# Optimization experiments

Measured on AMD Instinct MI355X. Metric: run time of the kernel, lower is better.

## Reference

```python
import jax, jax.numpy as jnp
import numpy as np

N_NODES = 8192
N_EDGES = 65536
NB = 10            # number_of_basis
MID = 32           # middle_layer_size
MAX_R = 10.0       # max_radius
NZ, NM = 48, 16    # z / mol embedding sizes -> 64x0e node input
IN_S = NZ + NM     # 64 scalars
H_S, H_V = 32, 8   # hidden irreps 32x0e + 8x1o (dim 56)
O_S = 16           # output irreps 16x0e
W0N = IN_S * H_S + IN_S * H_V                                  # 2560
W1N = H_S*H_S + H_V*H_S + H_S*H_V + H_V*H_V + H_V*H_V          # 1664
W2N = H_S*O_S + H_V*O_S                                        # 640
H_DIM = H_S + 3 * H_V                                          # 56


def _fcnet(e, W1, W2):
    # e3nn FullyConnectedNet([NB, MID, numel], silu): fan-in normalized linears
    h = jax.nn.silu(e @ W1 / np.sqrt(W1.shape[0]))
    return h @ W2 / np.sqrt(W2.shape[0])


def _ln(x, g, b):
    m = jnp.mean(x, -1, keepdims=True)
    v = jnp.var(x, -1, keepdims=True)
    return (x - m) * jax.lax.rsqrt(v + 1e-5) * g + b


def _sus(t):
    # smooth compact-support bump helper: exp(-1/t) for t>0 else 0
    return jnp.where(t > 0, jnp.exp(-1.0 / jnp.where(t > 0, t, 1.0)), 0.0)


def _forward(pos, Ez, Em,
             b0_W1, b0_W2, b0_g, b0_b,
             b1_W1, b1_W2, b1_g, b1_b,
             b2_W1, b2_W2, b2_g, b2_b,
             z, mol_id, edge_src, edge_dst):
    N = pos.shape[0]
    E = edge_src.shape[0]
    avg = E / N  # avg_num_neighbors (static)

    # node embedding: 64x0e
    x = jnp.concatenate([Ez[z], Em[mol_id]], axis=-1)          # [N, 64]

    vec = pos[edge_dst] - pos[edge_src]                        # [E, 3]
    length = jnp.linalg.norm(vec, axis=1)                      # [E]

    # soft_one_hot_linspace(basis='smooth_finite', cutoff=True) * sqrt(NB)
    vals = jnp.linspace(0.0, MAX_R, NB + 2)[1:-1]
    step = MAX_R / (NB + 1)
    u = (length[:, None] - vals) / step
    emb = (1.14136 * np.exp(2.0)) * _sus(u + 1.0) * _sus(1.0 - u)
    emb = emb * np.sqrt(NB)                                    # [E, NB]

    # spherical harmonics lmax=1, normalize=True, 'component' norm
    nrm = vec / jnp.maximum(length, 1e-9)[:, None]
    sh_v = np.sqrt(3.0) * nrm                                  # [E, 3]  (l=1; l=0 comp == 1)

    # ---- interaction block 0: 64x0e -> 32x0e + 8x1o ----
    w = _fcnet(emb, b0_W1, b0_W2)                              # [E, 2560]
    w00 = w[:, :IN_S * H_S].reshape(E, IN_S, H_S)
    w01 = w[:, IN_S * H_S:].reshape(E, IN_S, H_V)
    xe = x[edge_src]                                           # [E, 64]
    es = jnp.einsum('eu,euw->ew', xe, w00) / np.sqrt(IN_S)
    ev = jnp.einsum('eu,euw,ei->ewi', xe, w01, sh_v) / np.sqrt(IN_S)
    msg = jnp.concatenate([es, ev.reshape(E, 3 * H_V)], -1)    # [E, 56]
    x = _ln(jax.ops.segment_sum(msg, edge_dst, num_segments=N) / np.sqrt(avg), b0_g, b0_b)

    # ---- interaction block 1: 32x0e+8x1o -> 32x0e+8x1o ----
    w = _fcnet(emb, b1_W1, b1_W2)                              # [E, 1664]
    o = 0
    w_ss  = w[:, o:o + H_S*H_S].reshape(E, H_S, H_S); o += H_S*H_S
    w_vvs = w[:, o:o + H_V*H_S].reshape(E, H_V, H_S); o += H_V*H_S
    w_sv  = w[:, o:o + H_S*H_V].reshape(E, H_S, H_V); o += H_S*H_V
    w_vs  = w[:, o:o + H_V*H_V].reshape(E, H_V, H_V); o += H_V*H_V
    w_vvv = w[:, o:o + H_V*H_V].reshape(E, H_V, H_V)
    xs = x[:, :H_S][edge_src]                                  # [E, 32]
    xv = x[:, H_S:].reshape(N, H_V, 3)[edge_src]               # [E, 8, 3]
    dot = jnp.einsum('eui,ei->eu', xv, sh_v) / np.sqrt(3.0)    # 1o x 1o -> 0e CG
    crs = jnp.cross(xv, sh_v[:, None, :]) / np.sqrt(2.0)       # 1o x 1o -> 1o CG
    es = (jnp.einsum('eu,euw->ew', xs, w_ss) / np.sqrt(H_S)
          + jnp.einsum('eu,euw->ew', dot, w_vvs) / np.sqrt(H_V)) / np.sqrt(2.0)
    ev = (jnp.einsum('eu,euw,ei->ewi', xs, w_sv, sh_v) / np.sqrt(H_S)
          + jnp.einsum('eui,euw->ewi', xv, w_vs) / np.sqrt(H_V)
          + jnp.einsum('eui,euw->ewi', crs, w_vvv) / np.sqrt(H_V)) / np.sqrt(3.0)
    msg = jnp.concatenate([es, ev.reshape(E, 3 * H_V)], -1)
    x = _ln(jax.ops.segment_sum(msg, edge_dst, num_segments=N) / np.sqrt(avg), b1_g, b1_b)

    # ---- interaction block 2: 32x0e+8x1o -> 16x0e ----
    w = _fcnet(emb, b2_W1, b2_W2)                              # [E, 640]
    w_ss  = w[:, :H_S * O_S].reshape(E, H_S, O_S)
    w_vvs = w[:, H_S * O_S:].reshape(E, H_V, O_S)
    xs = x[:, :H_S][edge_src]
    xv = x[:, H_S:].reshape(N, H_V, 3)[edge_src]
    dot = jnp.einsum('eui,ei->eu', xv, sh_v) / np.sqrt(3.0)
    es = (jnp.einsum('eu,euw->ew', xs, w_ss) / np.sqrt(H_S)
          + jnp.einsum('eu,euw->ew', dot, w_vvs) / np.sqrt(H_V)) / np.sqrt(2.0)
    x = _ln(jax.ops.segment_sum(es, edge_dst, num_segments=N) / np.sqrt(avg), b2_g, b2_b)
    return x                                                   # [N, 16]


def setup_inputs():
    key = jax.random.key(0)
    ks = jax.random.split(key, 16)
    edge_src = jax.random.randint(ks[3], (N_EDGES,), 0, N_NODES)
    # exclude self-loops (radius_graph never returns them)
    edge_dst = (edge_src + 1 + jax.random.randint(ks[4], (N_EDGES,), 0, N_NODES - 1)) % N_NODES
    return {
        'pos': jax.random.uniform(ks[0], (N_NODES, 3), jnp.float32) * 8.0,
        'z': jax.random.randint(ks[1], (N_NODES,), 0, 100),
        'mol_id': jax.random.randint(ks[2], (N_NODES,), 0, 2),
        'edge_src': edge_src,
        'edge_dst': edge_dst,
        'Ez': jax.random.normal(ks[5], (100, NZ), jnp.float32),
        'Em': jax.random.normal(ks[6], (2, NM), jnp.float32),
        'b0_W1': jax.random.normal(ks[7], (NB, MID), jnp.float32),
        'b0_W2': jax.random.normal(ks[8], (MID, W0N), jnp.float32),
        'b0_g': jnp.ones((H_DIM,), jnp.float32),
        'b0_b': jnp.zeros((H_DIM,), jnp.float32),
        'b1_W1': jax.random.normal(ks[9], (NB, MID), jnp.float32),
        'b1_W2': jax.random.normal(ks[10], (MID, W1N), jnp.float32),
        'b1_g': jnp.ones((H_DIM,), jnp.float32),
        'b1_b': jnp.zeros((H_DIM,), jnp.float32),
        'b2_W1': jax.random.normal(ks[11], (NB, MID), jnp.float32),
        'b2_W2': jax.random.normal(ks[12], (MID, W2N), jnp.float32),
        'b2_g': jnp.ones((O_S,), jnp.float32),
        'b2_b': jnp.zeros((O_S,), jnp.float32),
    }


def reference(pos, z, mol_id, edge_src, edge_dst, Ez, Em,
              b0_W1, b0_W2, b0_g, b0_b,
              b1_W1, b1_W2, b1_g, b1_b,
              b2_W1, b2_W2, b2_g, b2_b):
    return _forward(pos, Ez, Em,
                    b0_W1, b0_W2, b0_g, b0_b,
                    b1_W1, b1_W2, b1_g, b1_b,
                    b2_W1, b2_W2, b2_g, b2_b,
                    z, mol_id, edge_src, edge_dst)
```

## Files before the change

kernel.cpp:

```cpp
#include <hip/hip_runtime.h>

#define NNODES 8192
#define NEDGES 65536

#define K_PACK   0.02209708691f
#define K_P1SV   0.01804219593f
#define K_VVS    0.04419417382f
#define K_VS     0.03608439182f
#define K_VVV    0.02551551815f
#define K_DOT    0.57735026919f
#define K_PRELN  0.35355339059f
#define C_EMB    8.4335730689f

typedef unsigned int uint32;
typedef unsigned short ushort16;
typedef __attribute__((ext_vector_type(8))) short short8;
typedef __attribute__((ext_vector_type(4))) float floatx4;

__device__ __forceinline__ float siluf(float x) { return x / (1.0f + __expf(-x)); }
__device__ __forceinline__ float susf(float t) { return t > 0.0f ? __expf(-1.0f / t) : 0.0f; }
__device__ __forceinline__ ushort16 f2bf(float f) {
  uint32 u = __float_as_uint(f);
  return (ushort16)((u + 0x7fffu + ((u >> 16) & 1u)) >> 16);
}
__device__ __forceinline__ float bflo(uint32 v) { return __uint_as_float(v << 16); }
__device__ __forceinline__ float bfhi(uint32 v) { return __uint_as_float(v & 0xffff0000u); }
__device__ __forceinline__ float bfs(ushort16 v) { return __uint_as_float((uint32)v << 16); }

__global__ __launch_bounds__(256) void k_prep(
    const float* __restrict__ pos, const int* __restrict__ z, const int* __restrict__ mol,
    const int* __restrict__ esrc, const int* __restrict__ edst,
    const float* __restrict__ Ez, const float* __restrict__ Em,
    const float* __restrict__ W10, const float* __restrict__ W11, const float* __restrict__ W12,
    const float* __restrict__ W20, const float* __restrict__ W21, const float* __restrict__ W22,
    int* __restrict__ combo, ushort16* __restrict__ X0cb, float* __restrict__ sh,
    ushort16* __restrict__ h0b, ushort16* __restrict__ h1b, ushort16* __restrict__ h2b,
    ushort16* __restrict__ Bp0, ushort16* __restrict__ Bp1, ushort16* __restrict__ Bp2,
    ushort16* __restrict__ Bpw1, ushort16* __restrict__ Bpw2,
    int* __restrict__ deg, int* __restrict__ eidx) {
  __shared__ float Wl[320];
  int b = blockIdx.x;
  if (b < 768) {
    int which = b >> 8;
    int e = ((b & 255) << 8) + threadIdx.x;
    const float* W = (which == 0) ? W10 : (which == 1) ? W11 : W12;
    for (int i = threadIdx.x; i < 320; i += 256) Wl[i] = W[i];
    __syncthreads();
    int s = esrc[e], d = edst[e];
    float vx = pos[d * 3 + 0] - pos[s * 3 + 0];
    float vy = pos[d * 3 + 1] - pos[s * 3 + 1];
    float vz = pos[d * 3 + 2] - pos[s * 3 + 2];
    float len = sqrtf(vx * vx + vy * vy + vz * vz);
    if (which == 0) {
      int p = atomicAdd(&deg[d], 1);
      if (p < 64) eidx[(size_t)d * 64 + p] = e;
      float inv = 1.7320508076f / fmaxf(len, 1e-9f);
      sh[e * 3 + 0] = vx * inv; sh[e * 3 + 1] = vy * inv; sh[e * 3 + 2] = vz * inv;
    }
    float emb[10];
#pragma unroll
    for (int k = 0; k < 10; ++k) {
      float u = len * 1.1f - (float)(k + 1);
      emb[k] = C_EMB * susf(u + 1.0f) * susf(1.0f - u);
    }
    float H[32];
#pragma unroll
    for (int m = 0; m < 32; ++m) {
      float t = 0.f;
#pragma unroll
      for (int k = 0; k < 10; ++k) t += emb[k] * Wl[k * 32 + m];
      H[m] = siluf(t);
    }
    ushort16* hb = (which == 0) ? h0b : (which == 1) ? h1b : h2b;
    uint32* hp = (uint32*)(hb + (size_t)e * 32);
#pragma unroll
    for (int m = 0; m < 16; ++m)
      hp[m] = (uint32)f2bf(H[2 * m]) | ((uint32)f2bf(H[2 * m + 1]) << 16);
    return;
  }
  int idx = (b - 768) * 256 + threadIdx.x;
  if (idx < NNODES) { combo[idx] = z[idx] * 2 + mol[idx]; return; }
  idx -= NNODES;
  if (idx < 16384) {
    int c = idx >> 6, j = idx & 63;
    float v = 0.f;
    if (c < 200) {
      int zz = c >> 1, mm = c & 1;
      v = (j < 48) ? Ez[zz * 48 + j] : Em[mm * 16 + (j - 48)];
    }
    X0cb[idx] = f2bf(v);
    return;
  }
  idx -= 16384;
  if (idx < 81920) {
    int tile = idx >> 10; int r = idx & 1023;
    int kh = r >> 9; int rr = r & 511;
    int lane = rr >> 3, j = rr & 7;
    int k = kh * 32 + (lane >> 4) * 8 + j;
    int n = tile * 16 + (lane & 15);
    int c = n >> 5, m = n & 31;
    int col = (c < 32) ? (k * 32 + c) : (2048 + k * 8 + (c - 32));
    Bp0[idx] = f2bf(W20[m * 2560 + col] * K_PACK);
    return;
  }
  idx -= 81920;
  if (idx < 40960) {
    int tile = idx >> 9; int rr = idx & 511;
    int lane = rr >> 3, j = rr & 7;
    int k = (lane >> 4) * 8 + j;
    int n = tile * 16 + (lane & 15);
    int c = n >> 5, m = n & 31;
    float v = (c < 32) ? W21[m * 1664 + k * 32 + c] * K_PACK
                       : W21[m * 1664 + 1280 + k * 8 + (c - 32)] * K_P1SV;
    Bp1[idx] = f2bf(v);
    return;
  }
  idx -= 40960;
  if (idx < 16384) {
    int tile = idx >> 9; int rr = idx & 511;
    int lane = rr >> 3, j = rr & 7;
    int k = (lane >> 4) * 8 + j;
    int n = tile * 16 + (lane & 15);
    int c = n >> 5, m = n & 31;
    Bp2[idx] = f2bf(W22[m * 640 + k * 16 + c] * K_PACK);
    return;
  }
  idx -= 16384;
  if (idx < 12288) {
    int tile = idx >> 9; int rr = idx & 511;
    int lane = rr >> 3, j = rr & 7;
    int m = (lane >> 4) * 8 + j;
    int c = tile * 16 + (lane & 15);
    float v;
    if (c < 256) {
      int u = c >> 5, w = c & 31;
      v = W21[m * 1664 + 1024 + u * 32 + w] * K_VVS;
    } else {
      int r2 = c - 256; int t = r2 & 1; int l2 = r2 >> 1;
      int u = l2 >> 3, vv = l2 & 7;
      v = (t == 0) ? W21[m * 1664 + 1536 + u * 8 + vv] * K_VS
                   : W21[m * 1664 + 1600 + u * 8 + vv] * K_VVV;
    }
    Bpw1[idx] = f2bf(v);
    return;
  }
  idx -= 12288;
  {
    int tile = idx >> 9; int rr = idx & 511;
    int lane = rr >> 3, j = rr & 7;
    int m = (lane >> 4) * 8 + j;
    int c = tile * 16 + (lane & 15);
    int t = c & 1; int l2 = c >> 1;
    int u = l2 >> 3, wh = l2 & 7;
    Bpw2[idx] = f2bf(W22[m * 640 + 512 + u * 16 + wh * 2 + t] * K_VVS);
  }
}

__device__ __forceinline__ void gemm_tile(
    const ushort16* __restrict__ A, const ushort16* __restrict__ Bp, ushort16* __restrict__ C,
    int N, int K, int bx, int by, int wave, int lane) {
  int m0 = bx * 64 + wave * 16;
  int n0 = by * 64;
  int row = lane & 15, q = lane >> 4;
  int nkh = K >> 5;
  floatx4 acc[4];
  floatx4 zero = {0.f, 0.f, 0.f, 0.f};
#pragma unroll
  for (int t = 0; t < 4; ++t) acc[t] = zero;
  for (int kh = 0; kh < nkh; ++kh) {
    short8 a = *reinterpret_cast<const short8*>(A + (size_t)(m0 + row) * K + kh * 32 + q * 8);
#pragma unroll
    for (int t = 0; t < 4; ++t) {
      int T = (n0 >> 4) + t;
      short8 b = *reinterpret_cast<const short8*>(Bp + ((size_t)T * nkh + kh) * 512 + lane * 8);
      acc[t] = __builtin_amdgcn_mfma_f32_16x16x32_bf16(a, b, acc[t], 0, 0, 0);
    }
  }
  int colb = n0 + row;
#pragma unroll
  for (int t = 0; t < 4; ++t)
#pragma unroll
    for (int r = 0; r < 4; ++r)
      C[(size_t)(m0 + q * 4 + r) * N + colb + t * 16] = f2bf(acc[t][r]);
}

__global__ __launch_bounds__(256) void k_gemm_mfma(
    const ushort16* __restrict__ A, const ushort16* __restrict__ Bp, ushort16* __restrict__ C,
    int N, int K) {
  gemm_tile(A, Bp, C, N, K, blockIdx.x, blockIdx.y, threadIdx.x >> 6, threadIdx.x & 63);
}

__global__ __launch_bounds__(256) void k_msg0(
    const int* __restrict__ rowmap, const int* __restrict__ esrc,
    const float* __restrict__ sh, const ushort16* __restrict__ hb,
    const ushort16* __restrict__ Pb, ushort16* __restrict__ msg) {
  int e = __builtin_amdgcn_readfirstlane(blockIdx.x * 4 + (threadIdx.x >> 6));
  int lane = threadIdx.x & 63;
  int s = esrc[e];
  int row = rowmap[s];
  float sh0 = sh[e * 3 + 0], sh1 = sh[e * 3 + 1], sh2 = sh[e * 3 + 2];
  int c; float mult;
  if (lane < 32) { c = lane; mult = 1.0f; }
  else if (lane < 56) {
    int l = lane - 32; int v = l / 3; int i = l - v * 3;
    c = 32 + v;
    mult = (i == 0) ? sh0 : (i == 1 ? sh1 : sh2);
  } else { c = 0; mult = 0.0f; }
  const uint4* Hp = reinterpret_cast<const uint4*>(hb + (size_t)e * 32);
  const uint4* Pp = reinterpret_cast<const uint4*>(Pb + (size_t)row * 1280 + c * 32);
  float a = 0.f;
#pragma unroll
  for (int qq = 0; qq < 4; ++qq) {
    uint4 pv = Pp[qq];
    uint4 hv = Hp[qq];
    a += bflo(pv.x) * bflo(hv.x) + bfhi(pv.x) * bfhi(hv.x);
    a += bflo(pv.y) * bflo(hv.y) + bfhi(pv.y) * bfhi(hv.y);
    a += bflo(pv.z) * bflo(hv.z) + bfhi(pv.z) * bfhi(hv.z);
    a += bflo(pv.w) * bflo(hv.w) + bfhi(pv.w) * bfhi(hv.w);
  }
  if (lane < 56) msg[(size_t)e * 56 + lane] = f2bf(a * mult);
}

__global__ __launch_bounds__(256) void k_msg1f(
    const int* __restrict__ esrc, const float* __restrict__ sh, const ushort16* __restrict__ hb,
    const ushort16* __restrict__ Pb, const float* __restrict__ xv,
    const ushort16* __restrict__ Bpw, ushort16* __restrict__ msg) {
  __shared__ ushort16 Wlds[16][384];
  int w = threadIdx.x >> 6, lane = threadIdx.x & 63;
  int e0 = __builtin_amdgcn_readfirstlane(blockIdx.x * 16);
  int row = lane & 15, q = lane >> 4;
  short8 a1 = *reinterpret_cast<const short8*>(hb + (size_t)(e0 + row) * 32 + q * 8);
  floatx4 zero = {0.f, 0.f, 0.f, 0.f};
#pragma unroll
  for (int t6 = 0; t6 < 6; ++t6) {
    int T = w * 6 + t6;
    short8 b1 = *reinterpret_cast<const short8*>(Bpw + (size_t)T * 512 + lane * 8);
    floatx4 acc = __builtin_amdgcn_mfma_f32_16x16x32_bf16(a1, b1, zero, 0, 0, 0);
#pragma unroll
    for (int r = 0; r < 4; ++r)
      Wlds[q * 4 + r][T * 16 + row] = f2bf(acc[r]);
  }
  __syncthreads();
  int u = lane >> 3;
  int lv = lane - 32;
  int vq = (lv >= 0) ? ((lv / 3 > 7) ? 7 : lv / 3) : 0;
  int vi = (lv >= 0) ? (lv - (lv / 3) * 3) : 0;
  int bsrc = (lane < 32) ? (lane >> 2) : 0;
  int c; float multsel;
  if (lane < 32) c = lane;
  else c = 32 + vq;
#pragma unroll
  for (int k = 0; k < 4; ++k) {
    int e = e0 + w * 4 + k;
    int s = esrc[e];
    float sh0 = sh[e * 3 + 0], sh1 = sh[e * 3 + 1], sh2 = sh[e * 3 + 2];
    const float* xvp = xv + (size_t)s * 24 + u * 3;
    float x0 = xvp[0], x1 = xvp[1], x2 = xvp[2];
    float du = K_DOT * (x0 * sh0 + x1 * sh1 + x2 * sh2);
    float cr0 = x1 * sh2 - x2 * sh1;
    float cr1 = x2 * sh0 - x0 * sh2;
    float cr2 = x0 * sh1 - x1 * sh0;
    const ushort16* wp = &Wlds[w * 4 + k][0];
    uint2 wv = *reinterpret_cast<const uint2*>(wp + lane * 4);
    uint32 wsv = *reinterpret_cast<const uint32*>(wp + 256 + lane * 2);
    float b0 = du * bflo(wv.x), b1 = du * bfhi(wv.x);
    float b2 = du * bflo(wv.y), b3 = du * bfhi(wv.y);
    float avs = bflo(wsv), avv = bfhi(wsv);
    float e0v = x0 * avs + cr0 * avv;
    float e1v = x1 * avs + cr1 * avv;
    float e2v = x2 * avs + cr2 * avv;
#pragma unroll
    for (int off = 8; off < 64; off <<= 1) {
      b0 += __shfl_xor(b0, off, 64); b1 += __shfl_xor(b1, off, 64);
      b2 += __shfl_xor(b2, off, 64); b3 += __shfl_xor(b3, off, 64);
      e0v += __shfl_xor(e0v, off, 64); e1v += __shfl_xor(e1v, off, 64);
      e2v += __shfl_xor(e2v, off, 64);
    }
    float B0 = __shfl(b0, bsrc, 64), B1 = __shfl(b1, bsrc, 64);
    float B2 = __shfl(b2, bsrc, 64), B3 = __shfl(b3, bsrc, 64);
    float E0 = __shfl(e0v, vq, 64), E1 = __shfl(e1v, vq, 64), E2 = __shfl(e2v, vq, 64);
    float vterm, mult;
    if (lane < 32) {
      int j = lane & 3;
      vterm = (j == 0) ? B0 : (j == 1) ? B1 : (j == 2) ? B2 : B3;
      mult = 1.0f;
    } else {
      vterm = (vi == 0) ? E0 : (vi == 1) ? E1 : E2;
      mult = (vi == 0) ? sh0 : (vi == 1) ? sh1 : sh2;
    }
    const uint4* Hp = reinterpret_cast<const uint4*>(hb + (size_t)e * 32);
    const uint4* Pp = reinterpret_cast<const uint4*>(Pb + (size_t)s * 1280 + c * 32);
    float a = 0.f;
#pragma unroll
    for (int qq = 0; qq < 4; ++qq) {
      uint4 pv = Pp[qq];
      uint4 hv = Hp[qq];
      a += bflo(pv.x) * bflo(hv.x) + bfhi(pv.x) * bfhi(hv.x);
      a += bflo(pv.y) * bflo(hv.y) + bfhi(pv.y) * bfhi(hv.y);
      a += bflo(pv.z) * bflo(hv.z) + bfhi(pv.z) * bfhi(hv.z);
      a += bflo(pv.w) * bflo(hv.w) + bfhi(pv.w) * bfhi(hv.w);
    }
    if (lane < 56) msg[(size_t)e * 56 + lane] = f2bf(a * mult + vterm);
  }
}

__global__ __launch_bounds__(256) void k_msg2f(
    const int* __restrict__ esrc, const float* __restrict__ sh, const ushort16* __restrict__ hb,
    const ushort16* __restrict__ Pb, const float* __restrict__ xv,
    const ushort16* __restrict__ Bpw, ushort16* __restrict__ msg) {
  __shared__ ushort16 Wlds[16][128];
  int w = threadIdx.x >> 6, lane = threadIdx.x & 63;
  int e0 = __builtin_amdgcn_readfirstlane(blockIdx.x * 16);
  int row = lane & 15, q = lane >> 4;
  short8 a1 = *reinterpret_cast<const short8*>(hb + (size_t)(e0 + row) * 32 + q * 8);
  floatx4 zero = {0.f, 0.f, 0.f, 0.f};
#pragma unroll
  for (int t2 = 0; t2 < 2; ++t2) {
    int T = w * 2 + t2;
    short8 b1 = *reinterpret_cast<const short8*>(Bpw + (size_t)T * 512 + lane * 8);
    floatx4 acc = __builtin_amdgcn_mfma_f32_16x16x32_bf16(a1, b1, zero, 0, 0, 0);
#pragma unroll
    for (int r = 0; r < 4; ++r)
      Wlds[q * 4 + r][T * 16 + row] = f2bf(acc[r]);
  }
  __syncthreads();
  int u = lane >> 3;
  int wsrc = (lane & 15) >> 1;
#pragma unroll
  for (int k = 0; k < 4; ++k) {
    int e = e0 + w * 4 + k;
    int s = esrc[e];
    float sh0 = sh[e * 3 + 0], sh1 = sh[e * 3 + 1], sh2 = sh[e * 3 + 2];
    const float* xvp = xv + (size_t)s * 24 + u * 3;
    float du = K_DOT * (xvp[0] * sh0 + xvp[1] * sh1 + xvp[2] * sh2);
    uint32 w2 = *reinterpret_cast<const uint32*>(&Wlds[w * 4 + k][0] + lane * 2);
    float c0 = du * bflo(w2), c1 = du * bfhi(w2);
#pragma unroll
    for (int off = 8; off < 64; off <<= 1) {
      c0 += __shfl_xor(c0, off, 64); c1 += __shfl_xor(c1, off, 64);
    }
    float C0 = __shfl(c0, wsrc, 64), C1 = __shfl(c1, wsrc, 64);
    float vterm = ((lane & 1) == 0) ? C0 : C1;
    int qq = lane >> 4, wc = lane & 15;
    uint4 hv = reinterpret_cast<const uint4*>(hb + (size_t)e * 32)[qq];
    uint4 pv = reinterpret_cast<const uint4*>(Pb + (size_t)s * 512 + wc * 32)[qq];
    float a = bflo(pv.x) * bflo(hv.x) + bfhi(pv.x) * bfhi(hv.x)
            + bflo(pv.y) * bflo(hv.y) + bfhi(pv.y) * bfhi(hv.y)
            + bflo(pv.z) * bflo(hv.z) + bfhi(pv.z) * bfhi(hv.z)
            + bflo(pv.w) * bflo(hv.w) + bfhi(pv.w) * bfhi(hv.w);
    a += __shfl_xor(a, 16, 64);
    a += __shfl_xor(a, 32, 64);
    if (lane < 16) msg[(size_t)e * 16 + lane] = f2bf(a + vterm);
  }
}

__global__ __launch_bounds__(256) void k_gather_ln(
    const int* __restrict__ deg, const int* __restrict__ eidx,
    const ushort16* __restrict__ msg, int D,
    const float* __restrict__ g, const float* __restrict__ b,
    ushort16* __restrict__ xsb, float* __restrict__ xvf, float* __restrict__ outf) {
  int n = __builtin_amdgcn_readfirstlane(blockIdx.x * 4 + (threadIdx.x >> 6));
  int lane = threadIdx.x & 63;
  int cnt = deg[n]; if (cnt > 64) cnt = 64;
  const int* ep = eidx + (size_t)n * 64;
  float v = 0.f;
  for (int j = 0; j < cnt; ++j) {
    int e = ep[j];
    if (lane < D) v += bfs(msg[(size_t)e * D + lane]);
  }
  v *= K_PRELN;
  if (lane >= D) v = 0.f;
  float sm = v, sq = v * v;
#pragma unroll
  for (int off = 32; off > 0; off >>= 1) {
    sm += __shfl_xor(sm, off, 64);
    sq += __shfl_xor(sq, off, 64);
  }
  float invD = 1.0f / (float)D;
  float mean = sm * invD;
  float var = sq * invD - mean * mean;
  float rs = rsqrtf(var + 1e-5f);
  float r = (v - mean) * rs * g[lane < D ? lane : 0] + b[lane < D ? lane : 0];
  if (outf) {
    if (lane < D) outf[(size_t)n * D + lane] = r;
  } else {
    if (lane < 32) xsb[(size_t)n * 32 + lane] = f2bf(r);
    else if (lane < 56) xvf[(size_t)n * 24 + lane - 32] = r;
  }
}

extern "C" void kernel_launch(void* const* d_in, const int* in_sizes, int n_in,
                              void* d_out, int out_size, void* d_ws, size_t ws_size,
                              hipStream_t stream) {
  const float* pos = (const float*)d_in[0];
  const int* z = (const int*)d_in[1];
  const int* mol = (const int*)d_in[2];
  const int* esrc = (const int*)d_in[3];
  const int* edst = (const int*)d_in[4];
  const float* Ez = (const float*)d_in[5];
  const float* Em = (const float*)d_in[6];
  const float* b0W1 = (const float*)d_in[7];
  const float* b0W2 = (const float*)d_in[8];
  const float* b0g = (const float*)d_in[9];
  const float* b0b = (const float*)d_in[10];
  const float* b1W1 = (const float*)d_in[11];
  const float* b1W2 = (const float*)d_in[12];
  const float* b1g = (const float*)d_in[13];
  const float* b1b = (const float*)d_in[14];
  const float* b2W1 = (const float*)d_in[15];
  const float* b2W2 = (const float*)d_in[16];
  const float* b2g = (const float*)d_in[17];
  const float* b2b = (const float*)d_in[18];
  float* out = (float*)d_out;

  float* ws = (float*)d_ws;
  size_t o = 0;
  int* combo = (int*)(ws + o); o += NNODES;
  int* deg = (int*)(ws + o); o += NNODES;
  int* eidx = (int*)(ws + o); o += (size_t)NNODES * 64;
  ushort16* X0cb = (ushort16*)(ws + o); o += 8192;
  ushort16* xs1b = (ushort16*)(ws + o); o += 131072;
  float* xv1 = ws + o; o += (size_t)NNODES * 24;
  ushort16* h0b = (ushort16*)(ws + o); o += (size_t)NEDGES * 16;
  ushort16* h1b = (ushort16*)(ws + o); o += (size_t)NEDGES * 16;
  ushort16* h2b = (ushort16*)(ws + o); o += (size_t)NEDGES * 16;
  float* shb = ws + o; o += (size_t)NEDGES * 3;
  ushort16* Bp0 = (ushort16*)(ws + o); o += 40960;
  ushort16* Bp1 = (ushort16*)(ws + o); o += 20480;
  ushort16* Bp2 = (ushort16*)(ws + o); o += 8192;
  ushort16* Bpw1 = (ushort16*)(ws + o); o += 6144;
  ushort16* Bpw2 = (ushort16*)(ws + o); o += 2048;
  ushort16* P12 = (ushort16*)(ws + o); o += (size_t)NNODES * 640;
  ushort16* msgb = (ushort16*)(ws + o); o += (size_t)NEDGES * 28;

  ushort16* P0c = P12;
  ushort16* xs2b = xs1b;
  float* xv2 = xv1;
  ushort16* msg16 = msgb;

  hipMemsetAsync(deg, 0, NNODES * sizeof(int), stream);

  k_prep<<<1472, 256, 0, stream>>>(pos, z, mol, esrc, edst, Ez, Em,
                                   b0W1, b1W1, b2W1, b0W2, b1W2, b2W2,
                                   combo, X0cb, shb, h0b, h1b, h2b,
                                   Bp0, Bp1, Bp2, Bpw1, Bpw2, deg, eidx);

  k_gemm_mfma<<<dim3(4, 20), 256, 0, stream>>>(X0cb, Bp0, P0c, 1280, 64);
  k_msg0<<<16384, 256, 0, stream>>>(combo, esrc, shb, h0b, P0c, msgb);
  k_gather_ln<<<2048, 256, 0, stream>>>(deg, eidx, msgb, 56, b0g, b0b, xs1b, xv1, nullptr);

  k_gemm_mfma<<<dim3(128, 20), 256, 0, stream>>>(xs1b, Bp1, P12, 1280, 32);
  k_msg1f<<<4096, 256, 0, stream>>>(esrc, shb, h1b, P12, xv1, Bpw1, msgb);
  k_gather_ln<<<2048, 256, 0, stream>>>(deg, eidx, msgb, 56, b1g, b1b, xs2b, xv2, nullptr);

  k_gemm_mfma<<<dim3(128, 8), 256, 0, stream>>>(xs2b, Bp2, P12, 512, 32);
  k_msg2f<<<4096, 256, 0, stream>>>(esrc, shb, h2b, P12, xv2, Bpw2, msg16);
  k_gather_ln<<<2048, 256, 0, stream>>>(deg, eidx, msg16, 16, b2g, b2b, nullptr, nullptr, out);
}
```

Baseline: 223.3 us.

## Replace cross-lane shuffle reductions with per-lane u-loops over repacked weights

Repacks the per-edge vector weight tables so each output channel's eight u-weights are contiguous, then computes the vector terms in the message kernels with a per-lane loop over u using uniform (readfirstlane) source-node features. This removes the xor-shuffle reduction trees and broadcast shuffles. LDS rows are padded to reduce bank conflicts. The cost is more redundant scalar/VALU arithmetic per lane and more LDS reads per lane.

```diff
diff --git a/kernel.cpp b/kernel.cpp
--- a/kernel.cpp
+++ b/kernel.cpp
@@ -130,16 +130,17 @@
     int tile = idx >> 9; int rr = idx & 511;
     int lane = rr >> 3, j = rr & 7;
     int m = (lane >> 4) * 8 + j;
-    int c = tile * 16 + (lane & 15);
+    int n = tile * 16 + (lane & 15);
     float v;
-    if (c < 256) {
-      int u = c >> 5, w = c & 31;
-      v = W21[m * 1664 + 1024 + u * 32 + w] * K_VVS;
+    if (n < 256) {
+      int c = n >> 3, u = n & 7;
+      v = W21[m * 1664 + 1024 + u * 32 + c] * K_VVS;
+    } else if (n < 320) {
+      int vo = (n - 256) >> 3, u = n & 7;
+      v = W21[m * 1664 + 1536 + u * 8 + vo] * K_VS;
     } else {
-      int r2 = c - 256; int t = r2 & 1; int l2 = r2 >> 1;
-      int u = l2 >> 3, vv = l2 & 7;
-      v = (t == 0) ? W21[m * 1664 + 1536 + u * 8 + vv] * K_VS
-                   : W21[m * 1664 + 1600 + u * 8 + vv] * K_VVV;
+      int vo = (n - 320) >> 3, u = n & 7;
+      v = W21[m * 1664 + 1600 + u * 8 + vo] * K_VVV;
     }
     Bpw1[idx] = f2bf(v);
     return;
@@ -149,10 +150,9 @@
     int tile = idx >> 9; int rr = idx & 511;
     int lane = rr >> 3, j = rr & 7;
     int m = (lane >> 4) * 8 + j;
-    int c = tile * 16 + (lane & 15);
-    int t = c & 1; int l2 = c >> 1;
-    int u = l2 >> 3, wh = l2 & 7;
-    Bpw2[idx] = f2bf(W22[m * 640 + 512 + u * 16 + wh * 2 + t] * K_VVS);
+    int n = tile * 16 + (lane & 15);
+    int c = n >> 3, u = n & 7;
+    Bpw2[idx] = f2bf(W22[m * 640 + 512 + u * 16 + c] * K_VVS);
   }
 }
 
@@ -225,7 +225,7 @@
     const int* __restrict__ esrc, const float* __restrict__ sh, const ushort16* __restrict__ hb,
     const ushort16* __restrict__ Pb, const float* __restrict__ xv,
     const ushort16* __restrict__ Bpw, ushort16* __restrict__ msg) {
-  __shared__ ushort16 Wlds[16][384];
+  __shared__ ushort16 Wlds[16][392];
   int w = threadIdx.x >> 6, lane = threadIdx.x & 63;
   int e0 = __builtin_amdgcn_readfirstlane(blockIdx.x * 16);
   int row = lane & 15, q = lane >> 4;
@@ -241,52 +241,50 @@
       Wlds[q * 4 + r][T * 16 + row] = f2bf(acc[r]);
   }
   __syncthreads();
-  int u = lane >> 3;
   int lv = lane - 32;
   int vq = (lv >= 0) ? ((lv / 3 > 7) ? 7 : lv / 3) : 0;
   int vi = (lv >= 0) ? (lv - (lv / 3) * 3) : 0;
-  int bsrc = (lane < 32) ? (lane >> 2) : 0;
-  int c; float multsel;
-  if (lane < 32) c = lane;
-  else c = 32 + vq;
+  int c = (lane < 32) ? lane : 32 + vq;
 #pragma unroll
   for (int k = 0; k < 4; ++k) {
     int e = e0 + w * 4 + k;
-    int s = esrc[e];
+    int s = __builtin_amdgcn_readfirstlane(esrc[e]);
     float sh0 = sh[e * 3 + 0], sh1 = sh[e * 3 + 1], sh2 = sh[e * 3 + 2];
-    const float* xvp = xv + (size_t)s * 24 + u * 3;
-    float x0 = xvp[0], x1 = xvp[1], x2 = xvp[2];
-    float du = K_DOT * (x0 * sh0 + x1 * sh1 + x2 * sh2);
-    float cr0 = x1 * sh2 - x2 * sh1;
-    float cr1 = x2 * sh0 - x0 * sh2;
-    float cr2 = x0 * sh1 - x1 * sh0;
+    const float* xr = xv + (size_t)s * 24;
     const ushort16* wp = &Wlds[w * 4 + k][0];
-    uint2 wv = *reinterpret_cast<const uint2*>(wp + lane * 4);
-    uint32 wsv = *reinterpret_cast<const uint32*>(wp + 256 + lane * 2);
-    float b0 = du * bflo(wv.x), b1 = du * bfhi(wv.x);
-    float b2 = du * bflo(wv.y), b3 = du * bfhi(wv.y);
-    float avs = bflo(wsv), avv = bfhi(wsv);
-    float e0v = x0 * avs + cr0 * avv;
-    float e1v = x1 * avs + cr1 * avv;
-    float e2v = x2 * avs + cr2 * avv;
-#pragma unroll
-    for (int off = 8; off < 64; off <<= 1) {
-      b0 += __shfl_xor(b0, off, 64); b1 += __shfl_xor(b1, off, 64);
-      b2 += __shfl_xor(b2, off, 64); b3 += __shfl_xor(b3, off, 64);
-      e0v += __shfl_xor(e0v, off, 64); e1v += __shfl_xor(e1v, off, 64);
-      e2v += __shfl_xor(e2v, off, 64);
-    }
-    float B0 = __shfl(b0, bsrc, 64), B1 = __shfl(b1, bsrc, 64);
-    float B2 = __shfl(b2, bsrc, 64), B3 = __shfl(b3, bsrc, 64);
-    float E0 = __shfl(e0v, vq, 64), E1 = __shfl(e1v, vq, 64), E2 = __shfl(e2v, vq, 64);
     float vterm, mult;
     if (lane < 32) {
-      int j = lane & 3;
-      vterm = (j == 0) ? B0 : (j == 1) ? B1 : (j == 2) ? B2 : B3;
       mult = 1.0f;
+      uint4 wv = *reinterpret_cast<const uint4*>(wp + lane * 8);
+      float ww[8] = {bflo(wv.x), bfhi(wv.x), bflo(wv.y), bfhi(wv.y),
+                     bflo(wv.z), bfhi(wv.z), bflo(wv.w), bfhi(wv.w)};
+      vterm = 0.f;
+#pragma unroll
+      for (int u = 0; u < 8; ++u) {
+        float du = K_DOT * (xr[u * 3] * sh0 + xr[u * 3 + 1] * sh1 + xr[u * 3 + 2] * sh2);
+        vterm += du * ww[u];
+      }
     } else {
-      vterm = (vi == 0) ? E0 : (vi == 1) ? E1 : E2;
-      mult = (vi == 0) ? sh0 : (vi == 1) ? sh1 : sh2;
+      float shi = (vi == 0) ? sh0 : (vi == 1) ? sh1 : sh2;
+      float s1 = (vi == 0) ? sh1 : (vi == 1) ? sh2 : sh0;
+      float s2 = (vi == 0) ? sh2 : (vi == 1) ? sh0 : sh1;
+      mult = shi;
+      uint4 wvs = *reinterpret_cast<const uint4*>(wp + 256 + vq * 8);
+      uint4 wvv = *reinterpret_cast<const uint4*>(wp + 320 + vq * 8);
+      float vsw[8] = {bflo(wvs.x), bfhi(wvs.x), bflo(wvs.y), bfhi(wvs.y),
+                      bflo(wvs.z), bfhi(wvs.z), bflo(wvs.w), bfhi(wvs.w)};
+      float vvw[8] = {bflo(wvv.x), bfhi(wvv.x), bflo(wvv.y), bfhi(wvv.y),
+                      bflo(wvv.z), bfhi(wvv.z), bflo(wvv.w), bfhi(wvv.w)};
+      vterm = 0.f;
+#pragma unroll
+      for (int u = 0; u < 8; ++u) {
+        float xu0 = xr[u * 3], xu1 = xr[u * 3 + 1], xu2 = xr[u * 3 + 2];
+        float xui = (vi == 0) ? xu0 : (vi == 1) ? xu1 : xu2;
+        float xi1 = (vi == 0) ? xu1 : (vi == 1) ? xu2 : xu0;
+        float xi2 = (vi == 0) ? xu2 : (vi == 1) ? xu0 : xu1;
+        float crs = xi1 * s2 - xi2 * s1;
+        vterm += xui * vsw[u] + crs * vvw[u];
+      }
     }
     const uint4* Hp = reinterpret_cast<const uint4*>(hb + (size_t)e * 32);
     const uint4* Pp = reinterpret_cast<const uint4*>(Pb + (size_t)s * 1280 + c * 32);
@@ -308,7 +306,7 @@
     const int* __restrict__ esrc, const float* __restrict__ sh, const ushort16* __restrict__ hb,
     const ushort16* __restrict__ Pb, const float* __restrict__ xv,
     const ushort16* __restrict__ Bpw, ushort16* __restrict__ msg) {
-  __shared__ ushort16 Wlds[16][128];
+  __shared__ ushort16 Wlds[16][136];
   int w = threadIdx.x >> 6, lane = threadIdx.x & 63;
   int e0 = __builtin_amdgcn_readfirstlane(blockIdx.x * 16);
   int row = lane & 15, q = lane >> 4;
@@ -324,23 +322,22 @@
       Wlds[q * 4 + r][T * 16 + row] = f2bf(acc[r]);
   }
   __syncthreads();
-  int u = lane >> 3;
-  int wsrc = (lane & 15) >> 1;
+  int cch = lane & 15;
 #pragma unroll
   for (int k = 0; k < 4; ++k) {
     int e = e0 + w * 4 + k;
-    int s = esrc[e];
+    int s = __builtin_amdgcn_readfirstlane(esrc[e]);
     float sh0 = sh[e * 3 + 0], sh1 = sh[e * 3 + 1], sh2 = sh[e * 3 + 2];
-    const float* xvp = xv + (size_t)s * 24 + u * 3;
-    float du = K_DOT * (xvp[0] * sh0 + xvp[1] * sh1 + xvp[2] * sh2);
-    uint32 w2 = *reinterpret_cast<const uint32*>(&Wlds[w * 4 + k][0] + lane * 2);
-    float c0 = du * bflo(w2), c1 = du * bfhi(w2);
-#pragma unroll
-    for (int off = 8; off < 64; off <<= 1) {
-      c0 += __shfl_xor(c0, off, 64); c1 += __shfl_xor(c1, off, 64);
-    }
-    float C0 = __shfl(c0, wsrc, 64), C1 = __shfl(c1, wsrc, 64);
-    float vterm = ((lane & 1) == 0) ? C0 : C1;
+    const float* xr = xv + (size_t)s * 24;
+    uint4 wv = *reinterpret_cast<const uint4*>(&Wlds[w * 4 + k][0] + cch * 8);
+    float ww[8] = {bflo(wv.x), bfhi(wv.x), bflo(wv.y), bfhi(wv.y),
+                   bflo(wv.z), bfhi(wv.z), bflo(wv.w), bfhi(wv.w)};
+    float vterm = 0.f;
+#pragma unroll
+    for (int u = 0; u < 8; ++u) {
+      float du = K_DOT * (xr[u * 3] * sh0 + xr[u * 3 + 1] * sh1 + xr[u * 3 + 2] * sh2);
+      vterm += du * ww[u];
+    }
     int qq = lane >> 4, wc = lane & 15;
     uint4 hv = reinterpret_cast<const uint4*>(hb + (size_t)e * 32)[qq];
     uint4 pv = reinterpret_cast<const uint4*>(Pb + (size_t)s * 512 + wc * 32)[qq];
```

After: 220.9 us. Within noise of the previous version (-1.1%).
